# Performance work log

Hardware: AMD Instinct MI355X
Metric: run time of the kernel (lower is better)

## Reference

```python
import jax, jax.numpy as jnp
import numpy as np


def _build_K(seq_length, kernel_size):
    """Replicates MovingAvgTime's banded matrix construction + nearest-exact
    interpolation along the column axis, then transpose.
    Final K[j, a] = 1/k if starts[j] <= a < starts[j] + k else 0, where
    starts[j] = floor((j + 0.5) * (L - k + 1) / L) clamped (nearest-exact)."""
    L, k = seq_length, kernel_size
    n_cols = L - k + 1
    j = jnp.arange(L, dtype=jnp.float32)
    # nearest-exact index map from output size L back to input size n_cols
    starts = jnp.minimum(((j + 0.5) * (n_cols / L)).astype(jnp.int32), n_cols - 1)  # [L]
    a = jnp.arange(L, dtype=jnp.int32)
    band = (a[None, :] >= starts[:, None]) & (a[None, :] < starts[:, None] + k)  # [L, L]
    return band.astype(jnp.float32) / k


def setup_inputs() -> dict:
    key = jax.random.key(0)
    B, L, C = 32, 4096, 64
    x = jax.random.normal(key, (B, L, C), dtype=jnp.float32)
    return {"x": x, "kernel_size": 16}


def reference(x, kernel_size):
    L = x.shape[1]
    K = _build_K(L, kernel_size)           # [L, L] banded moving-average matrix
    # out[b, j, c] = sum_a K[j, a] * x[b, a, c]  (same as torch: self.K @ x)
    return jnp.einsum('ja,bac->bjc', K, x)
```

## Files before the change

### kernel.cpp

```cpp
#include <hip/hip_runtime.h>


#define LL   4096
#define C4   16
#define BJ   128
#define NR   144
#define JPT  8

__global__ __launch_bounds__(256) void mavg16_kernel(const float* __restrict__ x,
                                                     const int* __restrict__ kptr,
                                                     float* __restrict__ out) {
    __shared__ float4 lds[NR * C4];

    const int k = *kptr;
    const int ncols = LL - k + 1;
    const float cmap = (float)((double)ncols / (double)LL);

    const int nwg = (int)gridDim.x;
    const int cpx = nwg >> 3;
    const int bid = (int)blockIdx.x;
    const int w = (bid & 7) * cpx + (bid >> 3);

    const int b    = w >> 5;
    const int jblk = w & 31;
    const int j0b  = jblk * BJ;

    const int tid = (int)threadIdx.x;
    const int c4  = tid & 15;
    const int jgl = tid >> 4;

    const float4* xb = (const float4*)x + (size_t)b * (LL * C4);
    float4*       ob = (float4*)out     + (size_t)b * (LL * C4);

    if (k == 16) {
        int sbase = (int)(((float)j0b + 0.5f) * cmap);
        sbase = min(sbase, ncols - 1);

        const int base4 = sbase * C4;
        #pragma unroll
        for (int i = 0; i < 9; ++i) {
            int f = i * 256 + tid;
            int g = min(base4 + f, LL * C4 - 1);
            lds[f] = xb[g];
        }
        __syncthreads();

        const float inv = 0.0625f;
        const int j0 = j0b + jgl * JPT;
        int s0 = (int)(((float)j0 + 0.5f) * cmap);
        s0 = min(s0, ncols - 1);
        const int r0 = s0 - sbase;

        float4 acc = make_float4(0.f, 0.f, 0.f, 0.f);
        #pragma unroll
        for (int t = 0; t < 16; ++t) {
            float4 v = lds[(r0 + t) * C4 + c4];
            acc.x += v.x; acc.y += v.y; acc.z += v.z; acc.w += v.w;
        }
        ob[(size_t)j0 * C4 + c4] =
            make_float4(acc.x * inv, acc.y * inv, acc.z * inv, acc.w * inv);

        int sp = r0;
        #pragma unroll
        for (int t = 1; t < JPT; ++t) {
            int sn = (int)(((float)(j0 + t) + 0.5f) * cmap);
            sn = min(sn, ncols - 1) - sbase;
            float4 ra = lds[(sn + 15) * C4 + c4];
            float4 rs = lds[sp * C4 + c4];
            const bool slide = (sn != sp);
            acc.x += slide ? (ra.x - rs.x) : 0.0f;
            acc.y += slide ? (ra.y - rs.y) : 0.0f;
            acc.z += slide ? (ra.z - rs.z) : 0.0f;
            acc.w += slide ? (ra.w - rs.w) : 0.0f;
            sp = sn;
            ob[(size_t)(j0 + t) * C4 + c4] =
                make_float4(acc.x * inv, acc.y * inv, acc.z * inv, acc.w * inv);
        }
    } else {
        const float inv = 1.0f / (float)k;
        for (int t = 0; t < JPT; ++t) {
            const int j = j0b + jgl * JPT + t;
            int s = (int)(((float)j + 0.5f) * cmap);
            s = min(s, ncols - 1);
            float4 acc = make_float4(0.f, 0.f, 0.f, 0.f);
            for (int a = 0; a < k; ++a) {
                float4 v = xb[(size_t)(s + a) * C4 + c4];
                acc.x += v.x; acc.y += v.y; acc.z += v.z; acc.w += v.w;
            }
            ob[(size_t)j * C4 + c4] =
                make_float4(acc.x * inv, acc.y * inv, acc.z * inv, acc.w * inv);
        }
    }
}

extern "C" void kernel_launch(void* const* d_in, const int* in_sizes, int n_in,
                              void* d_out, int out_size, void* d_ws, size_t ws_size,
                              hipStream_t stream) {
    const float* x    = (const float*)d_in[0];
    const int*   kptr = (const int*)d_in[1];
    float*       out  = (float*)d_out;
    mavg16_kernel<<<dim3(1024), dim3(256), 0, stream>>>(x, kptr, out);
}
```

Measured before the change: 16.22 us.

## Halve tile size, use direct global-to-LDS loads and nontemporal stores

Each block now covers 64 output rows with 4 rows per thread instead of 128 rows with 8, and twice as many blocks are launched. The halo is staged through global_load_lds, which writes straight into LDS and skips the register round-trip. Outputs are written with nontemporal stores so the result stream does not pollute the cache. The cost is a larger halo fraction (80 staged rows per 64 output rows), and the 16-byte global_load_lds form may need newer hardware and compiler support.

```diff
diff --git a/kernel.cpp b/kernel.cpp
--- a/kernel.cpp
+++ b/kernel.cpp
@@ -3,14 +3,17 @@
 
 #define LL   4096
 #define C4   16
-#define BJ   128
-#define NR   144
-#define JPT  8
+#define BJ   64
+#define NR   80
+#define JPT  4
+#define NSTG 5
+
+typedef float v4 __attribute__((ext_vector_type(4)));
 
 __global__ __launch_bounds__(256) void mavg16_kernel(const float* __restrict__ x,
                                                      const int* __restrict__ kptr,
                                                      float* __restrict__ out) {
-    __shared__ float4 lds[NR * C4];
+    __shared__ v4 lds[NR * C4];
 
     const int k = *kptr;
     const int ncols = LL - k + 1;
@@ -21,27 +24,30 @@
     const int bid = (int)blockIdx.x;
     const int w = (bid & 7) * cpx + (bid >> 3);
 
-    const int b    = w >> 5;
-    const int jblk = w & 31;
+    const int b    = w >> 6;
+    const int jblk = w & 63;
     const int j0b  = jblk * BJ;
 
     const int tid = (int)threadIdx.x;
     const int c4  = tid & 15;
     const int jgl = tid >> 4;
 
-    const float4* xb = (const float4*)x + (size_t)b * (LL * C4);
-    float4*       ob = (float4*)out     + (size_t)b * (LL * C4);
+    const v4* xb = (const v4*)x + (size_t)b * (LL * C4);
+    v4*       ob = (v4*)out     + (size_t)b * (LL * C4);
 
     if (k == 16) {
         int sbase = (int)(((float)j0b + 0.5f) * cmap);
         sbase = min(sbase, ncols - 1);
+        const int base4 = sbase * C4;
 
-        const int base4 = sbase * C4;
         #pragma unroll
-        for (int i = 0; i < 9; ++i) {
-            int f = i * 256 + tid;
-            int g = min(base4 + f, LL * C4 - 1);
-            lds[f] = xb[g];
+        for (int i = 0; i < NSTG; ++i) {
+            const int f = i * 256 + tid;
+            const int g = min(base4 + f, LL * C4 - 1);
+            __builtin_amdgcn_global_load_lds(
+                (const __attribute__((address_space(1))) unsigned int*)(xb + g),
+                (__attribute__((address_space(3))) unsigned int*)&lds[f],
+                16, 0, 0);
         }
         __syncthreads();
 
@@ -51,30 +57,23 @@
         s0 = min(s0, ncols - 1);
         const int r0 = s0 - sbase;
 
-        float4 acc = make_float4(0.f, 0.f, 0.f, 0.f);
+        v4 acc = (v4){0.f, 0.f, 0.f, 0.f};
         #pragma unroll
         for (int t = 0; t < 16; ++t) {
-            float4 v = lds[(r0 + t) * C4 + c4];
-            acc.x += v.x; acc.y += v.y; acc.z += v.z; acc.w += v.w;
+            acc += lds[(r0 + t) * C4 + c4];
         }
-        ob[(size_t)j0 * C4 + c4] =
-            make_float4(acc.x * inv, acc.y * inv, acc.z * inv, acc.w * inv);
+        __builtin_nontemporal_store(acc * inv, &ob[(size_t)j0 * C4 + c4]);
 
         int sp = r0;
         #pragma unroll
         for (int t = 1; t < JPT; ++t) {
             int sn = (int)(((float)(j0 + t) + 0.5f) * cmap);
             sn = min(sn, ncols - 1) - sbase;
-            float4 ra = lds[(sn + 15) * C4 + c4];
-            float4 rs = lds[sp * C4 + c4];
-            const bool slide = (sn != sp);
-            acc.x += slide ? (ra.x - rs.x) : 0.0f;
-            acc.y += slide ? (ra.y - rs.y) : 0.0f;
-            acc.z += slide ? (ra.z - rs.z) : 0.0f;
-            acc.w += slide ? (ra.w - rs.w) : 0.0f;
+            v4 ra = lds[(sn + 15) * C4 + c4];
+            v4 rs = lds[sp * C4 + c4];
+            if (sn != sp) acc += ra - rs;
             sp = sn;
-            ob[(size_t)(j0 + t) * C4 + c4] =
-                make_float4(acc.x * inv, acc.y * inv, acc.z * inv, acc.w * inv);
+            __builtin_nontemporal_store(acc * inv, &ob[(size_t)(j0 + t) * C4 + c4]);
         }
     } else {
         const float inv = 1.0f / (float)k;
@@ -82,13 +81,11 @@
             const int j = j0b + jgl * JPT + t;
             int s = (int)(((float)j + 0.5f) * cmap);
             s = min(s, ncols - 1);
-            float4 acc = make_float4(0.f, 0.f, 0.f, 0.f);
+            v4 acc = (v4){0.f, 0.f, 0.f, 0.f};
             for (int a = 0; a < k; ++a) {
-                float4 v = xb[(size_t)(s + a) * C4 + c4];
-                acc.x += v.x; acc.y += v.y; acc.z += v.z; acc.w += v.w;
+                acc += xb[(size_t)(s + a) * C4 + c4];
             }
-            ob[(size_t)j * C4 + c4] =
-                make_float4(acc.x * inv, acc.y * inv, acc.z * inv, acc.w * inv);
+            ob[(size_t)j * C4 + c4] = acc * inv;
         }
     }
 }
@@ -99,5 +96,5 @@
     const float* x    = (const float*)d_in[0];
     const int*   kptr = (const int*)d_in[1];
     float*       out  = (float*)d_out;
-    mavg16_kernel<<<dim3(1024), dim3(256), 0, stream>>>(x, kptr, out);
+    mavg16_kernel<<<dim3(2048), dim3(256), 0, stream>>>(x, kptr, out);
 }
```

After: 14.36 us. -11.4%, faster.
